# Kernel optimization log

Measured on AMD Instinct MI355X. Metric: run time of the kernel, lower is better.

The kernel has to match this reference:

```python
import jax, jax.numpy as jnp
import numpy as np

EMBED_DIM = 512
N_HEADS = 8
HEAD_DIM = EMBED_DIM // N_HEADS
MAX_GENES = 5000
SPARSITY_RATIO = 0.1
WINDOW = 20  # SparseAttention local window


def make_sparse_mask(key):
    # local band |i-j| <= window//2, plus random connections, plus diagonal
    idx = jnp.arange(MAX_GENES)
    mask = jnp.abs(idx[:, None] - idx[None, :]) <= (WINDOW // 2)
    n_random = int(SPARSITY_RATIO * MAX_GENES * MAX_GENES)
    k1, k2 = jax.random.split(key)
    ri = jax.random.randint(k1, (n_random,), 0, MAX_GENES)
    rj = jax.random.randint(k2, (n_random,), 0, MAX_GENES)
    mask = mask.at[ri, rj].set(True)
    mask = mask.at[idx, idx].set(True)
    return mask  # bool [MAX_GENES, MAX_GENES]


def setup_inputs() -> dict:
    key = jax.random.key(0)
    ks = jax.random.split(key, 10)
    B, S, E = 1, 4096, EMBED_DIM
    x = jax.random.normal(ks[0], (B, S, E), dtype=jnp.float32)
    init = lambda k: jax.random.normal(k, (E, E), dtype=jnp.float32) * 0.02
    return {
        "x": x,
        "Wq": init(ks[1]), "bq": jnp.zeros((E,), jnp.float32),
        "Wk": init(ks[2]), "bk": jnp.zeros((E,), jnp.float32),
        "Wv": init(ks[3]), "bv": jnp.zeros((E,), jnp.float32),
        "Wo": init(ks[4]), "bo": jnp.zeros((E,), jnp.float32),
        "mask": make_sparse_mask(ks[5]),
    }


def reference(x, Wq, bq, Wk, bk, Wv, bv, Wo, bo, mask):
    B, S, E = x.shape
    H, D = N_HEADS, HEAD_DIM
    # QKV projections (torch Linear: x @ W.T + b), split heads -> [B,H,S,D]
    Q = (x @ Wq.T + bq).reshape(B, S, H, D).transpose(0, 2, 1, 3)
    K = (x @ Wk.T + bk).reshape(B, S, H, D).transpose(0, 2, 1, 3)
    V = (x @ Wv.T + bv).reshape(B, S, H, D).transpose(0, 2, 1, 3)
    scale = 1.0 / jnp.sqrt(jnp.asarray(D, dtype=jnp.float32))
    scores = jnp.einsum('bhsd,bhtd->bhst', Q, K) * scale
    m = mask[:S, :S]  # static sparse pattern
    # original: scores*mask then masked_fill(mask==0, -inf) -> equivalent where
    scores = jnp.where(m[None, None], scores, -jnp.inf)
    w = jax.nn.softmax(scores, axis=-1)
    w = jnp.nan_to_num(w, nan=0.0)  # diag is always unmasked, but keep faithful
    out = jnp.einsum('bhst,bhtd->bhsd', w, V)
    out = out.transpose(0, 2, 1, 3).reshape(B, S, E)
    return out @ Wo.T + bo
```

## Files before the change

kernel.cpp:

```cpp
#include <hip/hip_runtime.h>
#include <hip/hip_bf16.h>
#include <stdint.h>

#define S 4096
#define E 512
#define H 8
#define D 64
#define MROW 5000

typedef __hip_bfloat16 bf16;
typedef __attribute__((ext_vector_type(8))) short bf16x8;
typedef __attribute__((ext_vector_type(4))) float f32x4;

#define CMUL (0.125f * 1.4426950408889634f)

__global__ __launch_bounds__(256) void prep(
    const void* __restrict__ mask, unsigned long long* __restrict__ bitsT,
    const float* __restrict__ x,  const float* __restrict__ wq,
    const float* __restrict__ wk, const float* __restrict__ wv,
    const float* __restrict__ wo, const float* __restrict__ bq,
    const float* __restrict__ bk, const float* __restrict__ bv,
    const float* __restrict__ bo,
    bf16* __restrict__ xb, bf16* __restrict__ wcat, bf16* __restrict__ wob,
    bf16* __restrict__ bcat, bf16* __restrict__ bob)
{
    const int tid = threadIdx.x;
    const int b   = blockIdx.x;
    const int gid = b * 256 + tid;
    for (int g = gid; g < 786944; g += 524288) {
        const float* src; bf16* dst; int e;
        if (g < 524288) { src = x; dst = xb; e = g * 4; }
        else {
            int r = g - 524288;
            if      (r < 65536)  { src = wq; dst = wcat;          e = r * 4; }
            else if (r < 131072) { src = wk; dst = wcat + 262144; e = (r - 65536) * 4; }
            else if (r < 196608) { src = wv; dst = wcat + 524288; e = (r - 131072) * 4; }
            else if (r < 262144) { src = wo; dst = wob;           e = (r - 196608) * 4; }
            else if (r < 262272) { src = bq; dst = bcat;          e = (r - 262144) * 4; }
            else if (r < 262400) { src = bk; dst = bcat + 512;    e = (r - 262272) * 4; }
            else if (r < 262528) { src = bv; dst = bcat + 1024;   e = (r - 262400) * 4; }
            else                 { src = bo; dst = bob;           e = (r - 262528) * 4; }
        }
        float4 v = *(const float4*)(src + e);
        union { bf16 h[4]; uint2 u; } cv;
        cv.h[0] = (bf16)v.x; cv.h[1] = (bf16)v.y;
        cv.h[2] = (bf16)v.z; cv.h[3] = (bf16)v.w;
        *(uint2*)(dst + e) = cv.u;
    }
    {
        const unsigned int* mw32 = (const unsigned int*)mask;
        int lane = tid & 63;
        int hit = 0;
#pragma unroll
        for (int i = 0; i < 8; ++i) {
            unsigned int w = mw32[lane + i * 64];
            if (w > 1u && (w & 0xFEFEFEFEu) == 0u) hit = 1;
        }
        const bool isbyte = (__ballot(hit) != 0ull);
        int wid  = (b * 256 + tid) >> 6;
        int nwav = (2048 * 256) >> 6;
        int total = (S / 64) * S;
        for (int w = wid; w < total; w += nwav) {
            int word = w >> 12;
            int row  = w & (S - 1);
            int col  = word * 64 + lane;
            unsigned int v;
            if (isbyte) v = ((const unsigned char*)mask)[(size_t)row * MROW + col];
            else        v = ((const unsigned int*)mask)[(size_t)row * MROW + col];
            unsigned long long bb = __ballot(v != 0u);
            if (lane == 0) bitsT[(size_t)word * S + row] = bb;
        }
    }
}

__global__ __launch_bounds__(256) void gemm_qkv(const bf16* __restrict__ A,
                                                const bf16* __restrict__ W,
                                                const bf16* __restrict__ bias,
                                                bf16* __restrict__ out)
{
    __shared__ bf16 As[64][72];
    __shared__ bf16 Bs[64][72];
    const int tid  = threadIdx.x;
    const int wid  = tid >> 6, lane = tid & 63;
    const int quad = lane >> 4, l15 = lane & 15;
    const int nbase = blockIdx.x * 64;
    const int mbase = blockIdx.y * 64;
    const int m0 = wid * 16;

    f32x4 acc[4];
#pragma unroll
    for (int i = 0; i < 4; ++i) acc[i] = (f32x4){0.f, 0.f, 0.f, 0.f};

    for (int kt = 0; kt < E / 64; ++kt) {
        const int kb = kt * 64;
        __syncthreads();
#pragma unroll
        for (int i = 0; i < 2; ++i) {
            int slot = tid + i * 256;
            int row = slot >> 3, kg = slot & 7;
            *(uint4*)&As[row][kg * 8] = *(const uint4*)&A[(size_t)(mbase + row) * E + kb + kg * 8];
            *(uint4*)&Bs[row][kg * 8] = *(const uint4*)&W[(size_t)(nbase + row) * E + kb + kg * 8];
        }
        __syncthreads();
        bf16x8 a0 = *(bf16x8*)&As[m0 + l15][quad * 8];
        bf16x8 a1 = *(bf16x8*)&As[m0 + l15][32 + quad * 8];
#pragma unroll
        for (int nt = 0; nt < 4; ++nt) {
            bf16x8 b0 = *(bf16x8*)&Bs[nt * 16 + l15][quad * 8];
            bf16x8 b1 = *(bf16x8*)&Bs[nt * 16 + l15][32 + quad * 8];
            acc[nt] = __builtin_amdgcn_mfma_f32_16x16x32_bf16(a0, b0, acc[nt], 0, 0, 0);
            acc[nt] = __builtin_amdgcn_mfma_f32_16x16x32_bf16(a1, b1, acc[nt], 0, 0, 0);
        }
    }
#pragma unroll
    for (int nt = 0; nt < 4; ++nt) {
        int col = nbase + nt * 16 + l15;
        float bv = (float)bias[col];
#pragma unroll
        for (int r = 0; r < 4; ++r) {
            int row = mbase + m0 + quad * 4 + r;
            float v = acc[nt][r] + bv;
            int t = col >> 9, hh = (col >> 6) & 7, d = col & 63;
            if (t == 0) v *= CMUL;
            out[((size_t)t * H + hh) * S * D + (size_t)row * D + d] = (bf16)v;
        }
    }
}

__global__ __launch_bounds__(256) void attn(const bf16* __restrict__ Qp,
                                            const bf16* __restrict__ Kp,
                                            const bf16* __restrict__ Vp,
                                            const unsigned long long* __restrict__ bitsT,
                                            float* __restrict__ Opart,
                                            float* __restrict__ Lpart,
                                            int ktper)
{
    __shared__ __align__(16) char smem[32768];
    bf16 (*Ps)[32][64] = (bf16(*)[32][64])smem;
    bf16 (*Ks)[64]     = (bf16(*)[64])(smem + 16384);
    bf16 (*Vts)[64]    = (bf16(*)[64])(smem + 24576);

    const int tid  = threadIdx.x;
    const int wid  = tid >> 6, lane = tid & 63;
    const int quad = lane >> 4, l15 = lane & 15;
    const int qb = blockIdx.x, h = blockIdx.y, split = blockIdx.z;
    const int qbase = qb * 128;
    const int m0 = wid * 32;
    const bf16* Qh = Qp + (size_t)h * S * D;
    const bf16* Kh = Kp + (size_t)h * S * D;
    const bf16* Vh = Vp + (size_t)h * S * D;

    const int krow0 = tid >> 3, kkg = tid & 7;
    const int krow1 = (tid + 256) >> 3;
    const int ksw0 = (kkg ^ (krow0 & 7)) * 8;
    const int ksw1 = (kkg ^ (krow1 & 7)) * 8;
    const int vt0 = (tid & 31) * 2, vd0 = (tid >> 5) * 8;

    const bf16* qr0 = Qh + (size_t)(qbase + m0 + l15) * D;
    bf16x8 aq00 = *(const bf16x8*)(qr0 + quad * 8);
    bf16x8 aq01 = *(const bf16x8*)(qr0 + 32 + quad * 8);
    bf16x8 aq10 = *(const bf16x8*)(qr0 + 16 * D + quad * 8);
    bf16x8 aq11 = *(const bf16x8*)(qr0 + 16 * D + 32 + quad * 8);

    bf16x8 bl;
    {
        union { short s; bf16 b; } one; one.b = (bf16)1.0f;
        short v = (l15 == 0) ? one.s : (short)0;
#pragma unroll
        for (int j = 0; j < 8; ++j) bl[j] = v;
    }

    f32x4 o[4][2];
#pragma unroll
    for (int dt = 0; dt < 4; ++dt)
#pragma unroll
        for (int u = 0; u < 2; ++u) o[dt][u] = (f32x4){0.f, 0.f, 0.f, 0.f};
    f32x4 accl[2];
    accl[0] = (f32x4){0.f, 0.f, 0.f, 0.f};
    accl[1] = (f32x4){0.f, 0.f, 0.f, 0.f};

    const int kt0 = split * ktper;
    const int kt1 = min(S / 64, kt0 + ktper);

    const bf16* kp0 = Kh + (size_t)(kt0 * 64 + krow0) * D + kkg * 8;
    const bf16* kp1 = Kh + (size_t)(kt0 * 64 + krow1) * D + kkg * 8;
    const bf16* vp0 = Vh + (size_t)(kt0 * 64 + vt0) * D + vd0;
    const bf16* vp1 = Vh + (size_t)(kt0 * 64 + vt0 + 1) * D + vd0;
    uint4 kq0 = *(const uint4*)kp0;
    uint4 kq1 = *(const uint4*)kp1;
    uint4 vq0 = *(const uint4*)vp0;
    uint4 vq1 = *(const uint4*)vp1;

    const unsigned long long* mb0 = bitsT + (size_t)kt0 * S + qbase + m0 + l15;
    const unsigned long long* mb1 = mb0 + 16;

    const int ksw_rd = (l15 & 7);
    const float RB = 0.002816949f;
#pragma unroll 1
    for (int kt = kt0; kt < kt1; ++kt) {
        __syncthreads();
        *(uint4*)&Ks[krow0][ksw0] = kq0;
        *(uint4*)&Ks[krow1][ksw1] = kq1;
        {
            const unsigned int* w0 = (const unsigned int*)&vq0;
            const unsigned int* w1 = (const unsigned int*)&vq1;
#pragma unroll
            for (int j = 0; j < 8; ++j) {
                unsigned int pk = __builtin_amdgcn_perm(
                    w1[j >> 1], w0[j >> 1],
                    (j & 1) ? 0x07060302u : 0x05040100u);
                *(unsigned int*)&Vts[vd0 + j][vt0 ^ (j * 8)] = pk;
            }
        }
        if (kt + 1 < kt1) {
            kp0 += 64 * D; kp1 += 64 * D; vp0 += 64 * D; vp1 += 64 * D;
            kq0 = *(const uint4*)kp0;
            kq1 = *(const uint4*)kp1;
            vq0 = *(const uint4*)vp0;
            vq1 = *(const uint4*)vp1;
        }
        unsigned long long mw0 = *mb0; mb0 += S;
        unsigned long long mw1 = *mb1; mb1 += S;
        __syncthreads();

        f32x4 sc[2][4];
        {
            f32x4 z = (f32x4){RB, RB, RB, RB};
            __builtin_amdgcn_s_setprio(1);
#pragma unroll
            for (int nt = 0; nt < 4; ++nt) {
                bf16x8 kb0 = *(bf16x8*)&Ks[nt * 16 + l15][(quad ^ ksw_rd) * 8];
                bf16x8 kb1 = *(bf16x8*)&Ks[nt * 16 + l15][((quad + 4) ^ ksw_rd) * 8];
                sc[0][nt] = __builtin_amdgcn_mfma_f32_16x16x32_bf16(kb0, aq00, z, 0, 0, 0);
                sc[0][nt] = __builtin_amdgcn_mfma_f32_16x16x32_bf16(kb1, aq01, sc[0][nt], 0, 0, 0);
                sc[1][nt] = __builtin_amdgcn_mfma_f32_16x16x32_bf16(kb0, aq10, z, 0, 0, 0);
                sc[1][nt] = __builtin_amdgcn_mfma_f32_16x16x32_bf16(kb1, aq11, sc[1][nt], 0, 0, 0);
            }
            __builtin_amdgcn_s_setprio(0);
        }
#pragma unroll
        for (int half = 0; half < 2; ++half) {
#pragma unroll
            for (int u = 0; u < 2; ++u) {
                const unsigned long long sh = (u ? mw1 : mw0) >> (quad * 4);
                const unsigned int wlo = (unsigned int)sh;
                const unsigned int whi = (unsigned int)(sh >> 32);
#pragma unroll
                for (int ntl = 0; ntl < 2; ++ntl) {
                    const int nt = half * 2 + ntl;
                    const unsigned int wsel = (nt < 2) ? wlo : whi;
                    unsigned int a[4];
#pragma unroll
                    for (int r = 0; r < 4; ++r) {
                        const int bit = (nt & 1) * 16 + r;
                        unsigned int m = (unsigned int)((int)(wsel << (31 - bit)) >> 31);
                        a[r] = __float_as_uint(__builtin_amdgcn_exp2f(sc[u][nt][r])) & m;
                    }
                    uint2 pk;
                    pk.x = __builtin_amdgcn_perm(a[1], a[0], 0x07060302u);
                    pk.y = __builtin_amdgcn_perm(a[3], a[2], 0x07060302u);
                    *(uint2*)&Ps[wid][u * 16 + l15][(nt * 16 + quad * 4) ^ (ksw_rd * 8)] = pk;
                }
            }
            const int cu = ((quad + half * 4) ^ ksw_rd) * 8;
            bf16x8 ap0 = *(bf16x8*)&Ps[wid][l15][(quad * 8 + half * 32) ^ (ksw_rd * 8)];
            bf16x8 ap1 = *(bf16x8*)&Ps[wid][16 + l15][(quad * 8 + half * 32) ^ (ksw_rd * 8)];
            __builtin_amdgcn_s_setprio(1);
            accl[0] = __builtin_amdgcn_mfma_f32_16x16x32_bf16(ap0, bl, accl[0], 0, 0, 0);
            accl[1] = __builtin_amdgcn_mfma_f32_16x16x32_bf16(ap1, bl, accl[1], 0, 0, 0);
#pragma unroll
            for (int dt = 0; dt < 4; ++dt) {
                bf16x8 bv = *(bf16x8*)&Vts[dt * 16 + l15][cu];
                o[dt][0] = __builtin_amdgcn_mfma_f32_16x16x32_bf16(ap0, bv, o[dt][0], 0, 0, 0);
                o[dt][1] = __builtin_amdgcn_mfma_f32_16x16x32_bf16(ap1, bv, o[dt][1], 0, 0, 0);
            }
            __builtin_amdgcn_s_setprio(0);
        }
    }
    float* Op = Opart + (size_t)(split * H + h) * S * D;
    float* Lp = Lpart + (size_t)(split * H + h) * S;
#pragma unroll
    for (int u = 0; u < 2; ++u)
#pragma unroll
        for (int r = 0; r < 4; ++r) {
            int row = qbase + m0 + u * 16 + quad * 4 + r;
            if (l15 == 0) Lp[row] = accl[u][r];
#pragma unroll
            for (int dt = 0; dt < 4; ++dt)
                Op[(size_t)row * D + dt * 16 + l15] = o[dt][u][r];
        }
}

__global__ __launch_bounds__(256) void combine(const float* __restrict__ Opart,
                                               const float* __restrict__ Lpart,
                                               bf16* __restrict__ Ab, int nsplit)
{
    const size_t oh = (size_t)H * S * D;
    int g = blockIdx.x * 256 + threadIdx.x;
    int row = g >> 6;
    int cg  = g & 63;
    int hh  = cg >> 3;
    int d0  = (cg & 7) * 8;
    size_t base = ((size_t)hh * S + row) * D + d0;
    float a[8] = {0.f, 0.f, 0.f, 0.f, 0.f, 0.f, 0.f, 0.f};
    float l = 0.f;
    for (int s = 0; s < nsplit; ++s) {
        float4 p0 = *(const float4*)(Opart + (size_t)s * oh + base);
        float4 p1 = *(const float4*)(Opart + (size_t)s * oh + base + 4);
        a[0] += p0.x; a[1] += p0.y; a[2] += p0.z; a[3] += p0.w;
        a[4] += p1.x; a[5] += p1.y; a[6] += p1.z; a[7] += p1.w;
        l += Lpart[(size_t)s * H * S + (size_t)hh * S + row];
    }
    float inv = (l > 0.f) ? 1.f / l : 0.f;
    union { bf16 hb[8]; uint4 u; } cv;
#pragma unroll
    for (int j = 0; j < 8; ++j) cv.hb[j] = (bf16)(a[j] * inv);
    *(uint4*)&Ab[(size_t)row * E + hh * 64 + d0] = cv.u;
}

__global__ __launch_bounds__(256) void gemm_out(const bf16* __restrict__ A,
                                                const bf16* __restrict__ W,
                                                const bf16* __restrict__ bias,
                                                float* __restrict__ out)
{
    __shared__ bf16 As[64][72];
    __shared__ bf16 Bs[64][72];
    const int tid  = threadIdx.x;
    const int wid  = tid >> 6, lane = tid & 63;
    const int quad = lane >> 4, l15 = lane & 15;
    const int nbase = blockIdx.x * 64;
    const int mbase = blockIdx.y * 64;
    const int m0 = wid * 16;

    f32x4 acc[4];
#pragma unroll
    for (int i = 0; i < 4; ++i) acc[i] = (f32x4){0.f, 0.f, 0.f, 0.f};

    for (int kt = 0; kt < E / 64; ++kt) {
        const int kb = kt * 64;
        __syncthreads();
#pragma unroll
        for (int i = 0; i < 2; ++i) {
            int slot = tid + i * 256;
            int row = slot >> 3, kg = slot & 7;
            *(uint4*)&As[row][kg * 8] = *(const uint4*)&A[(size_t)(mbase + row) * E + kb + kg * 8];
            *(uint4*)&Bs[row][kg * 8] = *(const uint4*)&W[(size_t)(nbase + row) * E + kb + kg * 8];
        }
        __syncthreads();
        bf16x8 a0 = *(bf16x8*)&As[m0 + l15][quad * 8];
        bf16x8 a1 = *(bf16x8*)&As[m0 + l15][32 + quad * 8];
#pragma unroll
        for (int nt = 0; nt < 4; ++nt) {
            bf16x8 b0 = *(bf16x8*)&Bs[nt * 16 + l15][quad * 8];
            bf16x8 b1 = *(bf16x8*)&Bs[nt * 16 + l15][32 + quad * 8];
            acc[nt] = __builtin_amdgcn_mfma_f32_16x16x32_bf16(a0, b0, acc[nt], 0, 0, 0);
            acc[nt] = __builtin_amdgcn_mfma_f32_16x16x32_bf16(a1, b1, acc[nt], 0, 0, 0);
        }
    }
#pragma unroll
    for (int nt = 0; nt < 4; ++nt) {
        int col = nbase + nt * 16 + l15;
        float bv = (float)bias[col];
#pragma unroll
        for (int r = 0; r < 4; ++r) {
            int row = mbase + m0 + quad * 4 + r;
            out[(size_t)row * E + col] = acc[nt][r] + bv;
        }
    }
}

extern "C" void kernel_launch(void* const* d_in, const int* in_sizes, int n_in,
                              void* d_out, int out_size, void* d_ws, size_t ws_size,
                              hipStream_t stream)
{
    char* ws = (char*)d_ws;
    const size_t MB = (size_t)1 << 20;
    bf16* Qw   = (bf16*)(ws + 0 * MB);
    bf16* Kw   = (bf16*)(ws + 4 * MB);
    bf16* Vw   = (bf16*)(ws + 8 * MB);
    bf16* Ab   = (bf16*)(ws + 12 * MB);
    unsigned long long* bitsT = (unsigned long long*)(ws + 16 * MB);
    bf16* xb   = (bf16*)(ws + 18 * MB);
    bf16* Wcat = (bf16*)(ws + 22 * MB);
    bf16* Wob  = (bf16*)(ws + 24 * MB);
    bf16* bcat = (bf16*)(ws + 25 * MB);
    bf16* bob  = (bf16*)(ws + 25 * MB + 8192);
    float* Opart = (float*)(ws + 26 * MB);

    int nsplit = (ws_size >= 68 * MB) ? 5 : (ws_size >= 59 * MB) ? 4 : 2;
    int ktper  = (S / 64 + nsplit - 1) / nsplit;
    float* Lpart = (float*)(ws + 26 * MB + (size_t)nsplit * 8 * MB);

    hipLaunchKernelGGL(prep, dim3(2048), dim3(256), 0, stream,
                       d_in[9], bitsT,
                       (const float*)d_in[0], (const float*)d_in[1],
                       (const float*)d_in[3], (const float*)d_in[5],
                       (const float*)d_in[7], (const float*)d_in[2],
                       (const float*)d_in[4], (const float*)d_in[6],
                       (const float*)d_in[8],
                       xb, Wcat, Wob, bcat, bob);
    hipLaunchKernelGGL(gemm_qkv, dim3(24, 64), dim3(256), 0, stream,
                       xb, Wcat, bcat, Qw);
    hipLaunchKernelGGL(attn, dim3(S / 128, H, nsplit), dim3(256), 0, stream,
                       Qw, Kw, Vw, bitsT, Opart, Lpart, ktper);
    hipLaunchKernelGGL(combine, dim3(1024), dim3(256), 0, stream,
                       Opart, Lpart, Ab, nsplit);
    hipLaunchKernelGGL(gemm_out, dim3(8, 64), dim3(256), 0, stream,
                       Ab, Wob, bob, (float*)d_out);
}
```

Baseline: 255.9 us.

## Add 8-wave 256-row attention kernel with six-way KV split

Adds an attention variant in which 512-thread blocks cover 256 query rows, so each K/V tile staged in shared memory is reused by eight waves instead of four. When the workspace is large enough it also raises the key split count to six. The aim is to halve K/V global loads and staging per query and to keep more CUs busy. In exchange it uses more shared memory per block, writes more partial outputs for the combine step, and only runs if the workspace is at least 76 MB.

After: 511.1 us. 99.7% more time.

```diff
diff --git a/kernel.cpp b/kernel.cpp
--- a/kernel.cpp
+++ b/kernel.cpp
@@ -127,6 +127,164 @@
     }
 }
 
+__global__ __launch_bounds__(512, 6) void attn8(const bf16* __restrict__ Qp,
+                                                const bf16* __restrict__ Kp,
+                                                const bf16* __restrict__ Vp,
+                                                const unsigned long long* __restrict__ bitsT,
+                                                float* __restrict__ Opart,
+                                                float* __restrict__ Lpart,
+                                                int ktper)
+{
+    __shared__ __align__(16) char smem[49152];
+    bf16 (*Ps)[32][64] = (bf16(*)[32][64])smem;
+    bf16 (*Ks)[64]     = (bf16(*)[64])(smem + 32768);
+    bf16 (*Vts)[64]    = (bf16(*)[64])(smem + 40960);
+
+    const int tid  = threadIdx.x;
+    const int wid  = tid >> 6, lane = tid & 63;
+    const int quad = lane >> 4, l15 = lane & 15;
+    const int qb = blockIdx.x, h = blockIdx.y, split = blockIdx.z;
+    const int qbase = qb * 256;
+    const int m0 = wid * 32;
+    const bf16* Qh = Qp + (size_t)h * S * D;
+    const bf16* Kh = Kp + (size_t)h * S * D;
+    const bf16* Vh = Vp + (size_t)h * S * D;
+
+    const int krow0 = tid >> 3, kkg = tid & 7;
+    const int ksw0 = (kkg ^ (krow0 & 7)) * 8;
+    const int vt0 = (tid & 31) * 2, vd0 = (tid >> 5) * 4;
+
+    const bf16* qr0 = Qh + (size_t)(qbase + m0 + l15) * D;
+    bf16x8 aq00 = *(const bf16x8*)(qr0 + quad * 8);
+    bf16x8 aq01 = *(const bf16x8*)(qr0 + 32 + quad * 8);
+    bf16x8 aq10 = *(const bf16x8*)(qr0 + 16 * D + quad * 8);
+    bf16x8 aq11 = *(const bf16x8*)(qr0 + 16 * D + 32 + quad * 8);
+
+    bf16x8 bl;
+    {
+        union { short s; bf16 b; } one; one.b = (bf16)1.0f;
+        short v = (l15 == 0) ? one.s : (short)0;
+#pragma unroll
+        for (int j = 0; j < 8; ++j) bl[j] = v;
+    }
+
+    f32x4 o[4][2];
+#pragma unroll
+    for (int dt = 0; dt < 4; ++dt)
+#pragma unroll
+        for (int u = 0; u < 2; ++u) o[dt][u] = (f32x4){0.f, 0.f, 0.f, 0.f};
+    f32x4 accl[2];
+    accl[0] = (f32x4){0.f, 0.f, 0.f, 0.f};
+    accl[1] = (f32x4){0.f, 0.f, 0.f, 0.f};
+
+    const int kt0 = split * ktper;
+    const int kt1 = min(S / 64, kt0 + ktper);
+
+    const bf16* kp0 = Kh + (size_t)(kt0 * 64 + krow0) * D + kkg * 8;
+    const bf16* vp0 = Vh + (size_t)(kt0 * 64 + vt0) * D + vd0;
+    const bf16* vp1 = Vh + (size_t)(kt0 * 64 + vt0 + 1) * D + vd0;
+    uint4 kq0 = *(const uint4*)kp0;
+    uint2 vq0 = *(const uint2*)vp0;
+    uint2 vq1 = *(const uint2*)vp1;
+
+    const unsigned long long* mb0 = bitsT + (size_t)kt0 * S + qbase + m0 + l15;
+    const unsigned long long* mb1 = mb0 + 16;
+
+    const int ksw_rd = (l15 & 7);
+    const float RB = 0.002816949f;
+#pragma unroll 1
+    for (int kt = kt0; kt < kt1; ++kt) {
+        __syncthreads();
+        *(uint4*)&Ks[krow0][ksw0] = kq0;
+        {
+            const unsigned int* w0 = (const unsigned int*)&vq0;
+            const unsigned int* w1 = (const unsigned int*)&vq1;
+#pragma unroll
+            for (int j = 0; j < 4; ++j) {
+                unsigned int pk = __builtin_amdgcn_perm(
+                    w1[j >> 1], w0[j >> 1],
+                    (j & 1) ? 0x07060302u : 0x05040100u);
+                *(unsigned int*)&Vts[vd0 + j][vt0 ^ ((((vd0 & 4) + j) & 7) * 8)] = pk;
+            }
+        }
+        if (kt + 1 < kt1) {
+            kp0 += 64 * D; vp0 += 64 * D; vp1 += 64 * D;
+            kq0 = *(const uint4*)kp0;
+            vq0 = *(const uint2*)vp0;
+            vq1 = *(const uint2*)vp1;
+        }
+        unsigned long long mw0 = *mb0; mb0 += S;
+        unsigned long long mw1 = *mb1; mb1 += S;
+        __syncthreads();
+
+        f32x4 sc[2][4];
+        {
+            f32x4 z = (f32x4){RB, RB, RB, RB};
+            __builtin_amdgcn_s_setprio(1);
+#pragma unroll
+            for (int nt = 0; nt < 4; ++nt) {
+                bf16x8 kb0 = *(bf16x8*)&Ks[nt * 16 + l15][(quad ^ ksw_rd) * 8];
+                bf16x8 kb1 = *(bf16x8*)&Ks[nt * 16 + l15][((quad + 4) ^ ksw_rd) * 8];
+                sc[0][nt] = __builtin_amdgcn_mfma_f32_16x16x32_bf16(kb0, aq00, z, 0, 0, 0);
+                sc[0][nt] = __builtin_amdgcn_mfma_f32_16x16x32_bf16(kb1, aq01, sc[0][nt], 0, 0, 0);
+                sc[1][nt] = __builtin_amdgcn_mfma_f32_16x16x32_bf16(kb0, aq10, z, 0, 0, 0);
+                sc[1][nt] = __builtin_amdgcn_mfma_f32_16x16x32_bf16(kb1, aq11, sc[1][nt], 0, 0, 0);
+            }
+            __builtin_amdgcn_s_setprio(0);
+        }
+#pragma unroll
+        for (int half = 0; half < 2; ++half) {
+#pragma unroll
+            for (int u = 0; u < 2; ++u) {
+                const unsigned long long sh = (u ? mw1 : mw0) >> (quad * 4);
+                const unsigned int wlo = (unsigned int)sh;
+                const unsigned int whi = (unsigned int)(sh >> 32);
+#pragma unroll
+                for (int ntl = 0; ntl < 2; ++ntl) {
+                    const int nt = half * 2 + ntl;
+                    const unsigned int wsel = (nt < 2) ? wlo : whi;
+                    unsigned int a[4];
+#pragma unroll
+                    for (int r = 0; r < 4; ++r) {
+                        const int bit = (nt & 1) * 16 + r;
+                        unsigned int m = (unsigned int)((int)(wsel << (31 - bit)) >> 31);
+                        a[r] = __float_as_uint(__builtin_amdgcn_exp2f(sc[u][nt][r])) & m;
+                    }
+                    uint2 pk;
+                    pk.x = __builtin_amdgcn_perm(a[1], a[0], 0x07060302u);
+                    pk.y = __builtin_amdgcn_perm(a[3], a[2], 0x07060302u);
+                    *(uint2*)&Ps[wid][u * 16 + l15][(nt * 16 + quad * 4) ^ (ksw_rd * 8)] = pk;
+                }
+            }
+            const int cu = ((quad + half * 4) ^ ksw_rd) * 8;
+            bf16x8 ap0 = *(bf16x8*)&Ps[wid][l15][(quad * 8 + half * 32) ^ (ksw_rd * 8)];
+            bf16x8 ap1 = *(bf16x8*)&Ps[wid][16 + l15][(quad * 8 + half * 32) ^ (ksw_rd * 8)];
+            __builtin_amdgcn_s_setprio(1);
+            accl[0] = __builtin_amdgcn_mfma_f32_16x16x32_bf16(ap0, bl, accl[0], 0, 0, 0);
+            accl[1] = __builtin_amdgcn_mfma_f32_16x16x32_bf16(ap1, bl, accl[1], 0, 0, 0);
+#pragma unroll
+            for (int dt = 0; dt < 4; ++dt) {
+                bf16x8 bv = *(bf16x8*)&Vts[dt * 16 + l15][cu];
+                o[dt][0] = __builtin_amdgcn_mfma_f32_16x16x32_bf16(ap0, bv, o[dt][0], 0, 0, 0);
+                o[dt][1] = __builtin_amdgcn_mfma_f32_16x16x32_bf16(ap1, bv, o[dt][1], 0, 0, 0);
+            }
+            __builtin_amdgcn_s_setprio(0);
+        }
+    }
+    float* Op = Opart + (size_t)(split * H + h) * S * D;
+    float* Lp = Lpart + (size_t)(split * H + h) * S;
+#pragma unroll
+    for (int u = 0; u < 2; ++u)
+#pragma unroll
+        for (int r = 0; r < 4; ++r) {
+            int row = qbase + m0 + u * 16 + quad * 4 + r;
+            if (l15 == 0) Lp[row] = accl[u][r];
+#pragma unroll
+            for (int dt = 0; dt < 4; ++dt)
+                Op[(size_t)row * D + dt * 16 + l15] = o[dt][u][r];
+        }
+}
+
 __global__ __launch_bounds__(256) void attn(const bf16* __restrict__ Qp,
                                             const bf16* __restrict__ Kp,
                                             const bf16* __restrict__ Vp,
@@ -387,7 +545,8 @@
     bf16* bob  = (bf16*)(ws + 25 * MB + 8192);
     float* Opart = (float*)(ws + 26 * MB);
 
-    int nsplit = (ws_size >= 68 * MB) ? 5 : (ws_size >= 59 * MB) ? 4 : 2;
+    const bool wide = (ws_size >= 76 * MB);
+    int nsplit = wide ? 6 : (ws_size >= 68 * MB) ? 5 : (ws_size >= 59 * MB) ? 4 : 2;
     int ktper  = (S / 64 + nsplit - 1) / nsplit;
     float* Lpart = (float*)(ws + 26 * MB + (size_t)nsplit * 8 * MB);
 
@@ -401,8 +560,12 @@
                        xb, Wcat, Wob, bcat, bob);
     hipLaunchKernelGGL(gemm_qkv, dim3(24, 64), dim3(256), 0, stream,
                        xb, Wcat, bcat, Qw);
-    hipLaunchKernelGGL(attn, dim3(S / 128, H, nsplit), dim3(256), 0, stream,
-                       Qw, Kw, Vw, bitsT, Opart, Lpart, ktper);
+    if (wide)
+        hipLaunchKernelGGL(attn8, dim3(S / 256, H, nsplit), dim3(512), 0, stream,
+                           Qw, Kw, Vw, bitsT, Opart, Lpart, ktper);
+    else
+        hipLaunchKernelGGL(attn, dim3(S / 128, H, nsplit), dim3(256), 0, stream,
+                           Qw, Kw, Vw, bitsT, Opart, Lpart, ktper);
     hipLaunchKernelGGL(combine, dim3(1024), dim3(256), 0, stream,
                        Opart, Lpart, Ab, nsplit);
     hipLaunchKernelGGL(gemm_out, dim3(8, 64), dim3(256), 0, stream,
```
